# Kernel tuning notes

Measured on AMD Instinct MI355X. Metric: run time of the kernel, lower is better.

## Reference

```python
import jax, jax.numpy as jnp
import numpy as np

D_MODEL = 768
NUM_HEADS = 12


def setup_inputs() -> dict:
    key = jax.random.key(0)
    ks = jax.random.split(key, 11)
    B, N, D = 4, 2048, D_MODEL
    s = 1.0 / np.sqrt(D)
    return {
        "q": jax.random.normal(ks[0], (B, N, D), jnp.float32),
        "k": jax.random.normal(ks[1], (B, N, D), jnp.float32),
        "v": jax.random.normal(ks[2], (B, N, D), jnp.float32),
        "wq": jax.random.normal(ks[3], (D, D), jnp.float32) * s,
        "bq": jnp.zeros((D,), jnp.float32),
        "wk": jax.random.normal(ks[4], (D, D), jnp.float32) * s,
        "bk": jnp.zeros((D,), jnp.float32),
        "wv": jax.random.normal(ks[5], (D, D), jnp.float32) * s,
        "bv": jnp.zeros((D,), jnp.float32),
        "wo": jax.random.normal(ks[6], (D, D), jnp.float32) * s,
        "bo": jnp.zeros((D,), jnp.float32),
    }


def _split_heads(x, num_heads):
    B, N, D = x.shape
    hd = D // num_heads
    return x.reshape(B, N, num_heads, hd).transpose(0, 2, 1, 3)  # (B,H,N,hd)


def reference(q, k, v, wq, bq, wk, bk, wv, bv, wo, bo):
    B, N, D = q.shape
    H = NUM_HEADS
    qw = q @ wq.T + bq
    kw = k @ wk.T + bk
    vw = v @ wv.T + bv
    hq = _split_heads(qw, H)
    hk = _split_heads(kw, H)
    hv = _split_heads(vw, H)
    scale = 1.0 / jnp.sqrt(jnp.asarray(hq.shape[-1], hq.dtype))
    scores = jnp.einsum("bhnd,bhmd->bhnm", hq, hk) * scale  # (B,H,N,N) explicit
    attn = jax.nn.softmax(scores, axis=-1)
    out = jnp.einsum("bhnm,bhmd->bhnd", attn, hv)
    out = out.transpose(0, 2, 1, 3).reshape(B, N, D)
    return out @ wo.T + bo
```

## Files before the change

### kernel.cpp

```cpp
#include <hip/hip_runtime.h>
#include <hip/hip_bf16.h>
#include <type_traits>


typedef __attribute__((ext_vector_type(8)))  __bf16 bf16x8;
typedef __attribute__((ext_vector_type(4)))  __bf16 bf16x4;
typedef __attribute__((ext_vector_type(4)))  float  f32x4;
typedef __attribute__((ext_vector_type(16))) float  f32x16;
typedef __attribute__((ext_vector_type(2)))  unsigned u32x2;
typedef __attribute__((ext_vector_type(4)))  unsigned u32x4;

#define NH  12
#define HD  64
#define DM  768
#define SEQ 2048
#define NB  4
#define M8  8192
#define ALPHA 0.18033688011112043f

__device__ __forceinline__ f32x4 mfma16(bf16x8 a, bf16x8 b, f32x4 c) {
  return __builtin_amdgcn_mfma_f32_16x16x32_bf16(a, b, c, 0, 0, 0);
}
__device__ __forceinline__ f32x16 mfma32(bf16x8 a, bf16x8 b, f32x16 c) {
  return __builtin_amdgcn_mfma_f32_32x32x16_bf16(a, b, c, 0, 0, 0);
}
__device__ __forceinline__ void gload16(const void* g, void* l) {
  auto gp = (__attribute__((address_space(1))) void*)(const_cast<void*>(g));
  auto lp = (__attribute__((address_space(3))) void*)(l);
  __builtin_amdgcn_global_load_lds(gp, lp, 16, 0, 0);
}
__device__ __forceinline__ float exp2_(float x) {
#if __has_builtin(__builtin_amdgcn_exp2f)
  return __builtin_amdgcn_exp2f(x);
#else
  return exp2f(x);
#endif
}

#define VMLG(n) do { asm volatile("s_waitcnt vmcnt(" #n ") lgkmcnt(0)" ::: "memory"); \
                     __builtin_amdgcn_sched_barrier(0); } while (0)
#define VMW(n) do { asm volatile("s_waitcnt vmcnt(" #n ")" ::: "memory"); \
                    __builtin_amdgcn_sched_barrier(0); } while (0)
#define BARX do { __builtin_amdgcn_s_barrier(); \
                  __builtin_amdgcn_sched_barrier(0); } while (0)

__device__ __forceinline__ u32x2 pswap(unsigned a, unsigned b) {
#if __has_builtin(__builtin_amdgcn_permlane32_swap)
  return __builtin_amdgcn_permlane32_swap(a, b, false, false);
#else
  u32x2 r;
  unsigned sa = (unsigned)__shfl_xor((int)a, 32), sb = (unsigned)__shfl_xor((int)b, 32);
  int hi = ((int)threadIdx.x >> 5) & 1;
  r[0] = hi ? sb : a;
  r[1] = hi ? b : sa;
  return r;
#endif
}
__device__ __forceinline__ unsigned f2u(float x) { return __builtin_bit_cast(unsigned, x); }
__device__ __forceinline__ float    u2f(unsigned x) { return __builtin_bit_cast(float, x); }
__device__ __forceinline__ float pcomb_sum(float v) {
  u32x2 r = pswap(f2u(v), f2u(v));
  return u2f(r[0]) + u2f(r[1]);
}
__device__ __forceinline__ unsigned pk(float lo, float hi_) {
  unsigned short ua = __builtin_bit_cast(unsigned short, (__bf16)lo);
  unsigned short ub = __builtin_bit_cast(unsigned short, (__bf16)hi_);
  return ((unsigned)ub << 16) | ua;
}

__global__ void cast4_kernel(const float* __restrict__ a, const float* __restrict__ b,
                             const float* __restrict__ c, const float* __restrict__ d,
                             __bf16* __restrict__ oa, __bf16* __restrict__ ob,
                             __bf16* __restrict__ oc, __bf16* __restrict__ od, int n4) {
  int y = blockIdx.y;
  const float* in = y == 0 ? a : y == 1 ? b : y == 2 ? c : d;
  __bf16* out     = y == 0 ? oa : y == 1 ? ob : y == 2 ? oc : od;
  const float sc  = y == 0 ? ALPHA : 1.0f;
  int i = blockIdx.x * 256 + threadIdx.x;
  if (i < n4) {
    float4 v = ((const float4*)in)[i];
    bf16x4 r;
    r[0] = (__bf16)(v.x * sc); r[1] = (__bf16)(v.y * sc);
    r[2] = (__bf16)(v.z * sc); r[3] = (__bf16)(v.w * sc);
    ((bf16x4*)out)[i] = r;
  }
}

__device__ __forceinline__ void proj_body(const float* __restrict__ A,
                                          const __bf16* __restrict__ B,
                                          const float* __restrict__ bias,
                                          __bf16* __restrict__ C,
                                          long m0, long n0, float bscale, bool trans) {
  __shared__ __align__(16) char LDSG[32768];
  const int tid = threadIdx.x;
  const int w = tid >> 6, l = tid & 63;
  const int g = l >> 4, i16 = l & 15;
  const int wr = w >> 1, wc = w & 1;
  const int srow = l >> 2;
  const int kq = l & 3;
  const int swc = kq ^ ((srow >> 1) & 3);

  const __bf16* Bg = B + (n0 + 16 * w + srow) * (long)DM + swc * 8;
  const float*  Ag = A + (m0 + 16 * w + srow) * (long)DM + kq * 8;
  char* const Awr = LDSG + w * 1024 + srow * 64 + swc * 16;

  const int chsw = (g ^ ((i16 >> 1) & 3)) * 16;
  const char* fA = LDSG + (wr * 64 + i16) * 64 + chsw;
  const char* fB = LDSG + 16384 + (wc * 64 + i16) * 64 + chsw;

  f32x4 acc[4][4] = {};
  float4 arA[4], arB[4];
  long kAa = 0, kAb = 32, kB = 0;

  auto LAA = [&]() {
    arA[0] = *(const float4*)(Ag + kAa);
    arA[1] = *(const float4*)(Ag + kAa + 4);
    arA[2] = *(const float4*)(Ag + 64 * (long)DM + kAa);
    arA[3] = *(const float4*)(Ag + 64 * (long)DM + kAa + 4);
    kAa += 64;
  };
  auto LAB = [&]() {
    arB[0] = *(const float4*)(Ag + kAb);
    arB[1] = *(const float4*)(Ag + kAb + 4);
    arB[2] = *(const float4*)(Ag + 64 * (long)DM + kAb);
    arB[3] = *(const float4*)(Ag + 64 * (long)DM + kAb + 4);
    kAb += 64;
  };
  auto SB = [&](int selb) {
    gload16(Bg + kB, LDSG + 16384 + selb + w * 1024);
    gload16(Bg + 64 * (long)DM + kB, LDSG + 16384 + selb + w * 1024 + 4096);
    kB += 32;
  };
  auto WAA = [&](int selb) {
    u32x4 u0, u1;
    u0[0] = pk(arA[0].x, arA[0].y); u0[1] = pk(arA[0].z, arA[0].w);
    u0[2] = pk(arA[1].x, arA[1].y); u0[3] = pk(arA[1].z, arA[1].w);
    u1[0] = pk(arA[2].x, arA[2].y); u1[1] = pk(arA[2].z, arA[2].w);
    u1[2] = pk(arA[3].x, arA[3].y); u1[3] = pk(arA[3].z, arA[3].w);
    *(u32x4*)(Awr + selb) = u0;
    *(u32x4*)(Awr + selb + 4096) = u1;
  };
  auto WAB = [&](int selb) {
    u32x4 u0, u1;
    u0[0] = pk(arB[0].x, arB[0].y); u0[1] = pk(arB[0].z, arB[0].w);
    u0[2] = pk(arB[1].x, arB[1].y); u0[3] = pk(arB[1].z, arB[1].w);
    u1[0] = pk(arB[2].x, arB[2].y); u1[1] = pk(arB[2].z, arB[2].w);
    u1[2] = pk(arB[3].x, arB[3].y); u1[3] = pk(arB[3].z, arB[3].w);
    *(u32x4*)(Awr + selb) = u0;
    *(u32x4*)(Awr + selb + 4096) = u1;
  };

#define PCOMPUTE(SELB) do { \
    bf16x8 af[4], bfr[4]; \
    _Pragma("unroll") for (int m = 0; m < 4; ++m) \
      af[m] = *(const bf16x8*)(fA + (SELB) + m * 1024); \
    _Pragma("unroll") for (int n = 0; n < 4; ++n) \
      bfr[n] = *(const bf16x8*)(fB + (SELB) + n * 1024); \
    __builtin_amdgcn_s_setprio(1); \
    _Pragma("unroll") for (int m = 0; m < 4; ++m) \
      _Pragma("unroll") for (int n = 0; n < 4; ++n) \
        acc[m][n] = mfma16(af[m], bfr[n], acc[m][n]); \
    __builtin_amdgcn_s_setprio(0); } while (0)

  SB(0); LAA(); LAB(); WAA(0);
  asm volatile("s_waitcnt lgkmcnt(0)" ::: "memory");
  __builtin_amdgcn_sched_barrier(0);
  BARX;
#pragma unroll 1
  for (int j = 0; j < 11; ++j) {
    SB(8192); LAA(); PCOMPUTE(0);    WAB(8192); VMLG(4); BARX;
    SB(0);    LAB(); PCOMPUTE(8192); WAA(0);    VMLG(4); BARX;
  }
  SB(8192); PCOMPUTE(0); WAB(8192); VMLG(0); BARX;
  PCOMPUTE(8192);
#undef PCOMPUTE

  if (trans) {
#pragma unroll
    for (int m = 0; m < 4; ++m)
#pragma unroll
      for (int n = 0; n < 4; ++n) {
        const long col = n0 + wc * 64 + n * 16 + i16;
        const float bv = bias[col] * bscale;
        const long row0 = m0 + wr * 64 + m * 16 + g * 4;
        bf16x4 v4;
#pragma unroll
        for (int r = 0; r < 4; ++r) v4[r] = (__bf16)(acc[m][n][r] + bv);
        *(bf16x4*)(C + col * (long)M8 + row0) = v4;
      }
  } else {
#pragma unroll
    for (int m = 0; m < 4; ++m)
#pragma unroll
      for (int n = 0; n < 4; ++n) {
        const long col = n0 + wc * 64 + n * 16 + i16;
        const float bv = bias[col] * bscale;
        const long row0 = m0 + wr * 64 + m * 16 + g * 4;
#pragma unroll
        for (int r = 0; r < 4; ++r)
          C[(row0 + r) * DM + col] = (__bf16)(acc[m][n][r] + bv);
      }
  }
}

__global__ __launch_bounds__(256, 3) void proj3_gemm(
    const float* __restrict__ q, const float* __restrict__ k, const float* __restrict__ v,
    const __bf16* __restrict__ wqb, const __bf16* __restrict__ wkb, const __bf16* __restrict__ wvb,
    const float* __restrict__ bq, const float* __restrict__ bk, const float* __restrict__ bv,
    __bf16* __restrict__ qpj, __bf16* __restrict__ kpj, __bf16* __restrict__ vpT) {
  const int gid = blockIdx.x;
  const int swz = (gid & 7) * 144 + (gid >> 3);
  const int z = swz / 384, rem = swz % 384;
  const long xb = rem / 6, yb = rem % 6;
  const float* A = z == 0 ? q : z == 1 ? k : v;
  const __bf16* B = z == 0 ? wqb : z == 1 ? wkb : wvb;
  const float* bias = z == 0 ? bq : z == 1 ? bk : bv;
  __bf16* C = z == 0 ? qpj : z == 1 ? kpj : vpT;
  proj_body(A, B, bias, C, xb * 128, yb * 128, z == 0 ? ALPHA : 1.0f, z == 2);
}

__global__ __launch_bounds__(256) void out_gemm(const __bf16* __restrict__ A,
                                                const __bf16* __restrict__ B,
                                                const float* __restrict__ bias,
                                                float* __restrict__ C) {
  const int gid = blockIdx.x;
  const int local = (gid >> 3);
  const long mt = (gid & 7) * 16 + local / 6;
  const long nt = local % 6;
  const long m0 = mt * 64, n0 = nt * 128;

  __shared__ __align__(16) char LDSG[24576];
  const int tid = threadIdx.x;
  const int w = tid >> 6, l = tid & 63;
  const int g = l >> 4, i16 = l & 15;
  const int wr = w >> 1, wc = w & 1;
  const int srow = l >> 2;
  const int swc = (l & 3) ^ ((srow >> 1) & 3);
  const __bf16* Ag = A + (m0 + 16 * w + srow) * (long)DM + swc * 8;
  const __bf16* Bg = B + (n0 + 16 * w + srow) * (long)DM + swc * 8;
  const int chsw = (g ^ ((i16 >> 1) & 3)) * 16;
  const char* fA = LDSG + (wr * 32 + i16) * 64 + chsw;
  const char* fB = LDSG + 8192 + (wc * 64 + i16) * 64 + chsw;

  f32x4 acc[2][4] = {};
  long kB = 0;

#define GSTAGE(S) do { \
    gload16(Ag + kB, LDSG + (S) * 4096 + w * 1024); \
    gload16(Bg + kB, LDSG + 8192 + (S) * 8192 + w * 1024); \
    gload16(Bg + 64 * (long)DM + kB, LDSG + 8192 + (S) * 8192 + w * 1024 + 4096); \
    kB += 32; } while (0)

#define GCOMPUTE(S) do { \
    bf16x8 af[2], bfr[4]; \
    _Pragma("unroll") for (int m = 0; m < 2; ++m) \
      af[m] = *(const bf16x8*)(fA + (S) * 4096 + m * 1024); \
    _Pragma("unroll") for (int n = 0; n < 4; ++n) \
      bfr[n] = *(const bf16x8*)(fB + (S) * 8192 + n * 1024); \
    __builtin_amdgcn_s_setprio(1); \
    _Pragma("unroll") for (int m = 0; m < 2; ++m) \
      _Pragma("unroll") for (int n = 0; n < 4; ++n) \
        acc[m][n] = mfma16(af[m], bfr[n], acc[m][n]); \
    __builtin_amdgcn_s_setprio(0); } while (0)

  GSTAGE(0); GSTAGE(1);
#pragma unroll 1
  for (int k = 0; k + 128 <= DM; k += 64) {
    VMW(3); BARX; GCOMPUTE(0); BARX; GSTAGE(0);
    VMW(3); BARX; GCOMPUTE(1); BARX; GSTAGE(1);
  }
  VMW(3); BARX; GCOMPUTE(0);
  VMW(0); BARX; GCOMPUTE(1);
#undef GSTAGE
#undef GCOMPUTE

#pragma unroll
  for (int m = 0; m < 2; ++m)
#pragma unroll
    for (int n = 0; n < 4; ++n) {
      const long col = n0 + wc * 64 + n * 16 + i16;
      const float bv = bias[col];
      const long row0 = m0 + wr * 32 + m * 16 + g * 4;
#pragma unroll
      for (int r = 0; r < 4; ++r)
        C[(row0 + r) * DM + col] = acc[m][n][r] + bv;
    }
}

__global__ __launch_bounds__(256, 3) void attn_fwd(const __bf16* __restrict__ qp,
                                                   const __bf16* __restrict__ kp,
                                                   const __bf16* __restrict__ vpT,
                                                   __bf16* __restrict__ ao) {
  __shared__ __align__(16) __bf16 Ks[2][64 * 64];
  __shared__ __align__(16) __bf16 Vs[2][64 * 64];

  const int wg = blockIdx.x;
  const int xcd = wg & 7;
  const int idx = wg >> 3;
  const int bh = xcd * 6 + (idx >> 4);
  const int qt = idx & 15;
  const int b = bh / NH, h = bh % NH;

  const int tid = threadIdx.x;
  const int w = tid >> 6, l = tid & 63;
  const int l31 = l & 31, hi = l >> 5;

  const long qrow = (long)b * SEQ + qt * 128 + w * 32 + l31;
  const __bf16* qb = qp + qrow * DM + h * HD;
  bf16x8 qf[4];
#pragma unroll
  for (int kk = 0; kk < 4; ++kk) qf[kk] = *(const bf16x8*)(qb + kk * 16 + hi * 8);

  f32x16 o0 = {}, o1 = {};
  float lsum = 0.f;
  bf16x8 vfp[8], pfp[4];

  const int srow = tid >> 3;
  const int schunk = (tid & 7) ^ (srow & 7);
  const __bf16* kbase = kp + ((long)b * SEQ) * DM + h * HD;
  const __bf16* vtb = vpT + (long)(h * HD) * M8 + (long)b * SEQ;

  auto stage = [&](int T, int sel) {
    const long kt = (long)T * 64;
    __bf16* Kd = &Ks[sel][(w * 8) * 64];
    __bf16* Vd = &Vs[sel][(w * 8) * 64];
    gload16(kbase + (kt + srow) * (long)DM + schunk * 8, Kd);
    gload16(kbase + (kt + 32 + srow) * (long)DM + schunk * 8, Kd + 32 * 64);
    gload16(vtb + (long)srow * M8 + kt + schunk * 8, Vd);
    gload16(vtb + (long)(32 + srow) * M8 + kt + schunk * 8, Vd + 32 * 64);
  };

  auto qk = [&](const __bf16* Kc, f32x16& s0, f32x16& s1, bool pv) {
    bf16x8 kf[8];
#pragma unroll
    for (int kk = 0; kk < 4; ++kk) {
      const int sw = ((kk * 2 + hi) ^ (l31 & 7)) * 8;
      kf[kk]     = *(const bf16x8*)&Kc[l31 * 64 + sw];
      kf[4 + kk] = *(const bf16x8*)&Kc[2048 + l31 * 64 + sw];
    }
    __builtin_amdgcn_s_setprio(1);
    if (pv) {
#pragma unroll
      for (int ks = 0; ks < 4; ++ks) {
        o0 = mfma32(vfp[ks], pfp[ks], o0);
        o1 = mfma32(vfp[4 + ks], pfp[ks], o1);
      }
    }
#pragma unroll
    for (int kk = 0; kk < 4; ++kk) {
      s0 = mfma32(kf[kk], qf[kk], s0);
      s1 = mfma32(kf[4 + kk], qf[kk], s1);
    }
    __builtin_amdgcn_s_setprio(0);
  };

  auto load_v = [&](const __bf16* Vc) {
#pragma unroll
    for (int ks = 0; ks < 4; ++ks) {
      const int sw = ((ks * 2 + hi) ^ (l31 & 7)) * 8;
      vfp[ks]     = *(const bf16x8*)&Vc[l31 * 64 + sw];
      vfp[4 + ks] = *(const bf16x8*)&Vc[2048 + l31 * 64 + sw];
    }
  };

  auto softmax_pack = [&](f32x16& s0, f32x16& s1) {
#pragma unroll
    for (int r = 0; r < 16; ++r) s0[r] = exp2_(s0[r]);
#pragma unroll
    for (int r = 0; r < 16; ++r) s1[r] = exp2_(s1[r]);
    f32x16 ps = s0 + s1;
    const float t0 = (ps[0] + ps[1]) + (ps[2] + ps[3]);
    const float t1 = (ps[4] + ps[5]) + (ps[6] + ps[7]);
    const float t2 = (ps[8] + ps[9]) + (ps[10] + ps[11]);
    const float t3 = (ps[12] + ps[13]) + (ps[14] + ps[15]);
    lsum += (t0 + t1) + (t2 + t3);
#pragma unroll
    for (int ks = 0; ks < 4; ++ks) {
      const int base = 8 * (ks & 1);
      const f32x16& S = (ks < 2) ? s0 : s1;
      unsigned pa = pk(S[base + 0], S[base + 1]);
      unsigned pc = pk(S[base + 2], S[base + 3]);
      unsigned pb = pk(S[base + 4], S[base + 5]);
      unsigned pd = pk(S[base + 6], S[base + 7]);
      u32x2 r02 = pswap(pa, pb);
      u32x2 r13 = pswap(pc, pd);
      u32x4 pw;
      pw[0] = r02[0]; pw[1] = r13[0]; pw[2] = r02[1]; pw[3] = r13[1];
      pfp[ks] = __builtin_bit_cast(bf16x8, pw);
    }
  };

  stage(0, 0);
  stage(1, 1);
  __syncthreads();
  {
    f32x16 s0 = {}, s1 = {};
    qk(&Ks[0][0], s0, s1, false);
    load_v(&Vs[0][0]);
    softmax_pack(s0, s1);
    __syncthreads();
  }
#pragma unroll 1
  for (int t = 1; t < SEQ / 64; ++t) {
    const int sel = t & 1;
    if (t + 1 < SEQ / 64) stage(t + 1, sel ^ 1);
    f32x16 s0 = {}, s1 = {};
    qk(&Ks[sel][0], s0, s1, true);
    load_v(&Vs[sel][0]);
    softmax_pack(s0, s1);
    __syncthreads();
  }
  {
    __builtin_amdgcn_s_setprio(1);
#pragma unroll
    for (int ks = 0; ks < 4; ++ks) {
      o0 = mfma32(vfp[ks], pfp[ks], o0);
      o1 = mfma32(vfp[4 + ks], pfp[ks], o1);
    }
    __builtin_amdgcn_s_setprio(0);
  }

  const float inv = 1.0f / pcomb_sum(lsum);
  __bf16* obase = ao + qrow * DM + h * HD;
#pragma unroll
  for (int rg = 0; rg < 4; ++rg) {
    bf16x4 v0, v1;
#pragma unroll
    for (int j = 0; j < 4; ++j) {
      v0[j] = (__bf16)(o0[rg * 4 + j] * inv);
      v1[j] = (__bf16)(o1[rg * 4 + j] * inv);
    }
    *(bf16x4*)(obase + 8 * rg + 4 * hi) = v0;
    *(bf16x4*)(obase + 32 + 8 * rg + 4 * hi) = v1;
  }
}

extern "C" void kernel_launch(void* const* d_in, const int* in_sizes, int n_in,
                              void* d_out, int out_size, void* d_ws, size_t ws_size,
                              hipStream_t stream) {
  const float* q  = (const float*)d_in[0];
  const float* k  = (const float*)d_in[1];
  const float* v  = (const float*)d_in[2];
  const float* wq = (const float*)d_in[3];
  const float* bq = (const float*)d_in[4];
  const float* wk = (const float*)d_in[5];
  const float* bk = (const float*)d_in[6];
  const float* wv = (const float*)d_in[7];
  const float* bv = (const float*)d_in[8];
  const float* wo = (const float*)d_in[9];
  const float* bo = (const float*)d_in[10];

  const long S = (long)M8 * DM;
  const long W = (long)DM * DM;
  __bf16* ws = (__bf16*)d_ws;
  __bf16 *wqb = ws, *wkb = wqb + W, *wvb = wkb + W, *wob = wvb + W;
  __bf16 *qpj = wob + W, *kpj = qpj + S, *vpT = kpj + S, *aob = vpT + S;

  cast4_kernel<<<dim3((unsigned)(W / 4 / 256), 4), 256, 0, stream>>>(
      wq, wk, wv, wo, wqb, wkb, wvb, wob, (int)(W / 4));

  proj3_gemm<<<1152, 256, 0, stream>>>(q, k, v, wqb, wkb, wvb, bq, bk, bv, qpj, kpj, vpT);

  attn_fwd<<<768, 256, 0, stream>>>(qpj, kpj, vpT, aob);

  out_gemm<<<768, 256, 0, stream>>>(aob, wob, bo, (float*)d_out);
}
```

Baseline: 148.5 us.

## Stage fp32 activations via direct LDS loads and compute softmax row sums with MFMA

The projection GEMM now copies fp32 A tiles straight into a larger swizzled LDS buffer with global_load_lds. It converts them to bf16 when reading fragments, replacing the register round-trip and packed LDS stores, and reorders the double-buffered pipeline to wait, barrier, compute, barrier, then issue the next loads. In the attention kernel, the softmax denominator is taken from an extra MFMA that multiplies P by a ones vector, replacing the scalar VALU reductions and the cross-lane sum. The cost is twice the A bytes in LDS, conversion work on every fragment read, and one extra MFMA per PV step.

```diff
diff --git a/kernel.cpp b/kernel.cpp
--- a/kernel.cpp
+++ b/kernel.cpp
@@ -37,8 +37,6 @@
 #endif
 }
 
-#define VMLG(n) do { asm volatile("s_waitcnt vmcnt(" #n ") lgkmcnt(0)" ::: "memory"); \
-                     __builtin_amdgcn_sched_barrier(0); } while (0)
 #define VMW(n) do { asm volatile("s_waitcnt vmcnt(" #n ")" ::: "memory"); \
                     __builtin_amdgcn_sched_barrier(0); } while (0)
 #define BARX do { __builtin_amdgcn_s_barrier(); \
@@ -55,12 +53,6 @@
   r[1] = hi ? b : sa;
   return r;
 #endif
-}
-__device__ __forceinline__ unsigned f2u(float x) { return __builtin_bit_cast(unsigned, x); }
-__device__ __forceinline__ float    u2f(unsigned x) { return __builtin_bit_cast(float, x); }
-__device__ __forceinline__ float pcomb_sum(float v) {
-  u32x2 r = pswap(f2u(v), f2u(v));
-  return u2f(r[0]) + u2f(r[1]);
 }
 __device__ __forceinline__ unsigned pk(float lo, float hi_) {
   unsigned short ua = __builtin_bit_cast(unsigned short, (__bf16)lo);
@@ -91,89 +83,61 @@
                                           const float* __restrict__ bias,
                                           __bf16* __restrict__ C,
                                           long m0, long n0, float bscale, bool trans) {
-  __shared__ __align__(16) char LDSG[32768];
+  __shared__ __align__(16) char LDSG[49152];
   const int tid = threadIdx.x;
   const int w = tid >> 6, l = tid & 63;
   const int g = l >> 4, i16 = l & 15;
   const int wr = w >> 1, wc = w & 1;
-  const int srow = l >> 2;
-  const int kq = l & 3;
-  const int swc = kq ^ ((srow >> 1) & 3);
-
-  const __bf16* Bg = B + (n0 + 16 * w + srow) * (long)DM + swc * 8;
-  const float*  Ag = A + (m0 + 16 * w + srow) * (long)DM + kq * 8;
-  char* const Awr = LDSG + w * 1024 + srow * 64 + swc * 16;
-
-  const int chsw = (g ^ ((i16 >> 1) & 3)) * 16;
-  const char* fA = LDSG + (wr * 64 + i16) * 64 + chsw;
-  const char* fB = LDSG + 16384 + (wc * 64 + i16) * 64 + chsw;
+
+  const int schA = (l & 7) ^ ((l >> 3) & 7);
+  const float* Ag = A + (m0 + w * 8 + (l >> 3)) * (long)DM + schA * 4;
+  const int srowB = l >> 2;
+  const int swcB = (l & 3) ^ ((srowB >> 1) & 3);
+  const __bf16* Bg = B + (n0 + 16 * w + srowB) * (long)DM + swcB * 8;
+
+  const int rsw = i16 & 7;
+  const char* pA0 = LDSG + (wr * 64 + i16) * 128 + (((2 * g) ^ rsw) * 16);
+  const char* pA1 = LDSG + (wr * 64 + i16) * 128 + ((((2 * g) ^ rsw) ^ 1) * 16);
+  const char* fB = LDSG + 32768 + (wc * 64 + i16) * 64 + (g ^ ((i16 >> 1) & 3)) * 16;
 
   f32x4 acc[4][4] = {};
-  float4 arA[4], arB[4];
-  long kAa = 0, kAb = 32, kB = 0;
-
-  auto LAA = [&]() {
-    arA[0] = *(const float4*)(Ag + kAa);
-    arA[1] = *(const float4*)(Ag + kAa + 4);
-    arA[2] = *(const float4*)(Ag + 64 * (long)DM + kAa);
-    arA[3] = *(const float4*)(Ag + 64 * (long)DM + kAa + 4);
-    kAa += 64;
-  };
-  auto LAB = [&]() {
-    arB[0] = *(const float4*)(Ag + kAb);
-    arB[1] = *(const float4*)(Ag + kAb + 4);
-    arB[2] = *(const float4*)(Ag + 64 * (long)DM + kAb);
-    arB[3] = *(const float4*)(Ag + 64 * (long)DM + kAb + 4);
-    kAb += 64;
-  };
-  auto SB = [&](int selb) {
-    gload16(Bg + kB, LDSG + 16384 + selb + w * 1024);
-    gload16(Bg + 64 * (long)DM + kB, LDSG + 16384 + selb + w * 1024 + 4096);
-    kB += 32;
-  };
-  auto WAA = [&](int selb) {
-    u32x4 u0, u1;
-    u0[0] = pk(arA[0].x, arA[0].y); u0[1] = pk(arA[0].z, arA[0].w);
-    u0[2] = pk(arA[1].x, arA[1].y); u0[3] = pk(arA[1].z, arA[1].w);
-    u1[0] = pk(arA[2].x, arA[2].y); u1[1] = pk(arA[2].z, arA[2].w);
-    u1[2] = pk(arA[3].x, arA[3].y); u1[3] = pk(arA[3].z, arA[3].w);
-    *(u32x4*)(Awr + selb) = u0;
-    *(u32x4*)(Awr + selb + 4096) = u1;
-  };
-  auto WAB = [&](int selb) {
-    u32x4 u0, u1;
-    u0[0] = pk(arB[0].x, arB[0].y); u0[1] = pk(arB[0].z, arB[0].w);
-    u0[2] = pk(arB[1].x, arB[1].y); u0[3] = pk(arB[1].z, arB[1].w);
-    u1[0] = pk(arB[2].x, arB[2].y); u1[1] = pk(arB[2].z, arB[2].w);
-    u1[2] = pk(arB[3].x, arB[3].y); u1[3] = pk(arB[3].z, arB[3].w);
-    *(u32x4*)(Awr + selb) = u0;
-    *(u32x4*)(Awr + selb + 4096) = u1;
-  };
-
-#define PCOMPUTE(SELB) do { \
+  long kk0 = 0;
+
+#define PSTAGE(SA, SB2) do { \
+    _Pragma("unroll") for (int j = 0; j < 4; ++j) \
+      gload16(Ag + (long)j * 32 * DM + kk0, LDSG + (SA) + (j * 32 + w * 8) * 128); \
+    gload16(Bg + kk0, LDSG + 32768 + (SB2) + w * 1024); \
+    gload16(Bg + 64 * (long)DM + kk0, LDSG + 32768 + (SB2) + w * 1024 + 4096); \
+    kk0 += 32; } while (0)
+
+#define PCOMP(SA, SB2) do { \
     bf16x8 af[4], bfr[4]; \
-    _Pragma("unroll") for (int m = 0; m < 4; ++m) \
-      af[m] = *(const bf16x8*)(fA + (SELB) + m * 1024); \
+    _Pragma("unroll") for (int m = 0; m < 4; ++m) { \
+      f32x4 lo = *(const f32x4*)(pA0 + (SA) + m * 2048); \
+      f32x4 hh = *(const f32x4*)(pA1 + (SA) + m * 2048); \
+      u32x4 u; \
+      u[0] = pk(lo[0], lo[1]); u[1] = pk(lo[2], lo[3]); \
+      u[2] = pk(hh[0], hh[1]); u[3] = pk(hh[2], hh[3]); \
+      af[m] = __builtin_bit_cast(bf16x8, u); \
+    } \
     _Pragma("unroll") for (int n = 0; n < 4; ++n) \
-      bfr[n] = *(const bf16x8*)(fB + (SELB) + n * 1024); \
+      bfr[n] = *(const bf16x8*)(fB + (SB2) + n * 1024); \
     __builtin_amdgcn_s_setprio(1); \
     _Pragma("unroll") for (int m = 0; m < 4; ++m) \
       _Pragma("unroll") for (int n = 0; n < 4; ++n) \
         acc[m][n] = mfma16(af[m], bfr[n], acc[m][n]); \
     __builtin_amdgcn_s_setprio(0); } while (0)
 
-  SB(0); LAA(); LAB(); WAA(0);
-  asm volatile("s_waitcnt lgkmcnt(0)" ::: "memory");
-  __builtin_amdgcn_sched_barrier(0);
-  BARX;
+  PSTAGE(0, 0); PSTAGE(16384, 8192);
 #pragma unroll 1
-  for (int j = 0; j < 11; ++j) {
-    SB(8192); LAA(); PCOMPUTE(0);    WAB(8192); VMLG(4); BARX;
-    SB(0);    LAB(); PCOMPUTE(8192); WAA(0);    VMLG(4); BARX;
-  }
-  SB(8192); PCOMPUTE(0); WAB(8192); VMLG(0); BARX;
-  PCOMPUTE(8192);
-#undef PCOMPUTE
+  for (int j2 = 0; j2 < 11; ++j2) {
+    VMW(6); BARX; PCOMP(0, 0);         BARX; PSTAGE(0, 0);
+    VMW(6); BARX; PCOMP(16384, 8192);  BARX; PSTAGE(16384, 8192);
+  }
+  VMW(6); BARX; PCOMP(0, 0);
+  VMW(0); BARX; PCOMP(16384, 8192);
+#undef PSTAGE
+#undef PCOMP
 
   if (trans) {
 #pragma unroll
@@ -311,8 +275,11 @@
 #pragma unroll
   for (int kk = 0; kk < 4; ++kk) qf[kk] = *(const bf16x8*)(qb + kk * 16 + hi * 8);
 
-  f32x16 o0 = {}, o1 = {};
-  float lsum = 0.f;
+  bf16x8 onesf;
+#pragma unroll
+  for (int j = 0; j < 8; ++j) onesf[j] = (__bf16)1.0f;
+
+  f32x16 o0 = {}, o1 = {}, lacc = {};
   bf16x8 vfp[8], pfp[4];
 
   const int srow = tid >> 3;
@@ -344,6 +311,7 @@
       for (int ks = 0; ks < 4; ++ks) {
         o0 = mfma32(vfp[ks], pfp[ks], o0);
         o1 = mfma32(vfp[4 + ks], pfp[ks], o1);
+        lacc = mfma32(onesf, pfp[ks], lacc);
       }
     }
 #pragma unroll
@@ -368,12 +336,6 @@
     for (int r = 0; r < 16; ++r) s0[r] = exp2_(s0[r]);
 #pragma unroll
     for (int r = 0; r < 16; ++r) s1[r] = exp2_(s1[r]);
-    f32x16 ps = s0 + s1;
-    const float t0 = (ps[0] + ps[1]) + (ps[2] + ps[3]);
-    const float t1 = (ps[4] + ps[5]) + (ps[6] + ps[7]);
-    const float t2 = (ps[8] + ps[9]) + (ps[10] + ps[11]);
-    const float t3 = (ps[12] + ps[13]) + (ps[14] + ps[15]);
-    lsum += (t0 + t1) + (t2 + t3);
 #pragma unroll
     for (int ks = 0; ks < 4; ++ks) {
       const int base = 8 * (ks & 1);
@@ -416,11 +378,12 @@
     for (int ks = 0; ks < 4; ++ks) {
       o0 = mfma32(vfp[ks], pfp[ks], o0);
       o1 = mfma32(vfp[4 + ks], pfp[ks], o1);
+      lacc = mfma32(onesf, pfp[ks], lacc);
     }
     __builtin_amdgcn_s_setprio(0);
   }
 
-  const float inv = 1.0f / pcomb_sum(lsum);
+  const float inv = 1.0f / lacc[0];
   __bf16* obase = ao + qrow * DM + h * HD;
 #pragma unroll
   for (int rg = 0; rg < 4; ++rg) {
```

After: 155.9 us. 5.0% more time.
